# Performance work log

Measured on AMD Instinct MI355X. Metric: run time of the kernel, lower is better.

The kernel has to match this reference:

```python
import jax, jax.numpy as jnp
import numpy as np

B, S, T, F, H, DEPTH = 8, 96, 96, 64, 64, 2


def setup_inputs() -> dict:
    key = jax.random.key(0)
    ks = jax.random.split(key, 10)
    scale = np.float32(1.0 / np.sqrt(H))
    rn = lambda k, sh: jax.random.normal(k, sh, dtype=jnp.float32)
    return {
        "src": rn(ks[0], (B, S, F)),
        "trg": rn(ks[1], (B, T, F)),
        "Wi_x": rn(ks[2], (DEPTH, F, H)) * scale,
        "Wh_x": rn(ks[3], (DEPTH, 2 * H, H)) * scale,
        "b_x": jnp.zeros((DEPTH, H), jnp.float32),
        "Wi_y": rn(ks[4], (DEPTH, F, H)) * scale,
        "Wh_y": rn(ks[5], (DEPTH, 2 * H, H)) * scale,
        "b_y": jnp.zeros((DEPTH, H), jnp.float32),
        "src_lens": jax.random.randint(ks[6], (B,), 1, S + 1),
        "trg_lens": jax.random.randint(ks[7], (B,), 1, T + 1),
    }


def _grid_layer(px, py, Whx, bx, Why, by):
    # px, py: (B, S, T, H) precomputed input projections (x @ Wi).
    # Wavefront recurrence: h_prev = [h_x(i-1,j), h_y(i,j-1)] (zeros at borders),
    # h_x(i,j) = tanh(px + h_prev @ Whx + bx), h_y(i,j) = tanh(py + h_prev @ Why + by).
    Bn, Sn, Tn, Hn = px.shape

    def row_step(hx_above_row, row_in):
        pxr, pyr = row_in  # (T, B, H) each

        def col_step(hy_left, col_in):
            pxc, pyc, hx_above = col_in  # (B, H) each
            h_prev = jnp.concatenate([hx_above, hy_left], axis=-1)  # (B, 2H)
            hx = jnp.tanh(pxc + h_prev @ Whx + bx)
            hy = jnp.tanh(pyc + h_prev @ Why + by)
            return hy, (hx, hy)

        _, (hx_row, hy_row) = jax.lax.scan(
            col_step, jnp.zeros((Bn, Hn), px.dtype), (pxr, pyr, hx_above_row))
        return hx_row, (hx_row, hy_row)

    px_t = jnp.transpose(px, (1, 2, 0, 3))  # (S, T, B, H)
    py_t = jnp.transpose(py, (1, 2, 0, 3))
    _, (hx, hy) = jax.lax.scan(
        row_step, jnp.zeros((Tn, Bn, Hn), px.dtype), (px_t, py_t))
    return jnp.transpose(hx, (2, 0, 1, 3)), jnp.transpose(hy, (2, 0, 1, 3))


def _forward(src, trg, Wi_x, Wh_x, b_x, Wi_y, Wh_y, b_y, src_lens, trg_lens):
    hx = hy = None
    hxs, hys = [], []
    for d in range(DEPTH):
        if d == 0:
            # depth 0: x input depends only on i, y input only on j
            px = jnp.broadcast_to((src @ Wi_x[0])[:, :, None, :], (B, S, T, H))
            py = jnp.broadcast_to((trg @ Wi_y[0])[:, None, :, :], (B, S, T, H))
        else:
            # depth d>0: inputs are previous depth's x/y outputs at the same (i,j)
            px = jnp.einsum('bsth,hk->bstk', hx, Wi_x[d])
            py = jnp.einsum('bsth,hk->bstk', hy, Wi_y[d])
        hx, hy = _grid_layer(px, py, Wh_x[d], b_x[d], Wh_y[d], b_y[d])
        hxs.append(hx)
        hys.append(hy)
    # zero out points outside each sample's (src_len x trg_len) valid grid
    mask = ((jnp.arange(S)[None, :, None] < src_lens[:, None, None])
            & (jnp.arange(T)[None, None, :] < trg_lens[:, None, None]))
    mask = mask[:, :, :, None].astype(src.dtype)  # (B, S, T, 1)
    out = jnp.stack([jnp.stack(hxs), jnp.stack(hys)])  # (2, DEPTH, B, S, T, H)
    return out * mask


_forward_jit = jax.jit(_forward)


def reference(src, trg, Wi_x, Wh_x, b_x, Wi_y, Wh_y, b_y, src_lens, trg_lens):
    return _forward_jit(src, trg, Wi_x, Wh_x, b_x, Wi_y, Wh_y, b_y,
                        src_lens, trg_lens)
```

## Files before the change

kernel.cpp:

```cpp
#include <hip/hip_runtime.h>

typedef unsigned short u16;
typedef unsigned int   u32;
typedef _Float16 f16x8 __attribute__((ext_vector_type(8)));
typedef float  f32x2  __attribute__((ext_vector_type(2)));
typedef float  f32x4  __attribute__((ext_vector_type(4)));
typedef int    i32x4  __attribute__((ext_vector_type(4)));
typedef u32    u32x2  __attribute__((ext_vector_type(2)));

#define Bn 8
#define Sn 96
#define Tn 96
#define Hn 64
#define H2n 128
#define STRB 152
#define ARRB 16384
#define STATEB 131072
#define PXROW 152
#define PXG   (Sn*PXROW)
#define PXBASE STATEB
#define LDSB  (STATEB + 2*PXG)
#define ODS 24320
#define TSTP 2432
#define TSCL 2.885390082f

__device__ __forceinline__ int imax(int a, int b){ return a > b ? a : b; }
__device__ __forceinline__ int imin(int a, int b){ return a < b ? a : b; }

__device__ __forceinline__ u32 pack2f16(float a, float b){
  _Float16 ha = (_Float16)a, hb = (_Float16)b;
  return (u32)__builtin_bit_cast(u16, ha) | ((u32)__builtin_bit_cast(u16, hb) << 16);
}
__device__ __forceinline__ float f16tof(u32 v){
  return (float)__builtin_bit_cast(_Float16, (u16)v);
}
__device__ __forceinline__ float fast_tanh_ps(float zp){
  float e = exp2f(zp);
  return __builtin_fmaf(-2.f, __builtin_amdgcn_rcpf(e + 1.f), 1.f);
}
__device__ __forceinline__ void barrier_lds_only(){
  asm volatile("s_waitcnt vmcnt(63) expcnt(7) lgkmcnt(0)\n\ts_barrier" ::: "memory");
}
__device__ __forceinline__ f16x8 ld_state(const char* p){
  u32x2 a = *(const u32x2*)(p);
  u32x2 b = *(const u32x2*)(p + 8);
  i32x4 v; v[0] = (int)a[0]; v[1] = (int)a[1]; v[2] = (int)b[0]; v[3] = (int)b[1];
  return __builtin_bit_cast(f16x8, v);
}

__global__ __launch_bounds__(64) void proj0_kernel(
  const float* __restrict__ src, const float* __restrict__ trg,
  const float* __restrict__ Wix, const float* __restrict__ Wiy,
  const float* __restrict__ bx, const float* __restrict__ by,
  float* __restrict__ ws)
{
  const int row = blockIdx.x, g = blockIdx.y, b = blockIdx.z;
  const int n = threadIdx.x;
  const float* x = (g == 0) ? (src + (b*Sn + row)*Hn) : (trg + (b*Tn + row)*Hn);
  const float* W = (g == 0) ? Wix : Wiy;
  float a = (g == 0) ? bx[n] : by[n];
  #pragma unroll 8
  for (int f = 0; f < Hn; ++f) a = fmaf(x[f], W[f*Hn + n], a);
  ws[((size_t)(b*2 + g)*Sn + row)*Hn + n] = a * TSCL;
}

__global__ __launch_bounds__(1024, 1) void grid_rnn_fused(
  const float* __restrict__ Whx, const float* __restrict__ Why,
  const float* __restrict__ Wix, const float* __restrict__ Wiy,
  const float* __restrict__ bx,  const float* __restrict__ by,
  const int* __restrict__ src_lens, const int* __restrict__ trg_lens,
  float* __restrict__ out, const float* __restrict__ ws)
{
  extern __shared__ u16 smem[];
  char* const smemc = (char*)smem;
  const int b    = blockIdx.x;
  const int tid  = threadIdx.x;
  const int lane = tid & 63;
  const int wid  = __builtin_amdgcn_readfirstlane(tid >> 6);
  const int q    = lane >> 4;
  const int c    = lane & 15;
  const int dep  = wid & 1;
  const int nh   = (wid >> 1) & 1;
  const int ch   = (wid >> 2) & 1;
  const int g    = wid >> 3;
  const int sl = __builtin_amdgcn_readfirstlane(src_lens[b]);
  const int tl = __builtin_amdgcn_readfirstlane(trg_lens[b]);
  const int NB = sl + tl;

  for (int idx = tid; idx < STATEB/16; idx += 1024) ((i32x4*)smem)[idx] = (i32x4)(0);

  {
    const int gp = tid >> 9;
    const int t5 = tid & 511;
    const float* wsg = ws + (size_t)(b*2 + gp)*Sn*Hn;
    #pragma unroll
    for (int it = 0; it < 6; ++it){
      int w = t5 + it*512;
      int row = w >> 5, pr = w & 31;
      f32x2 v = *(const f32x2*)(wsg + row*64 + pr*2);
      *(u32*)(smemc + PXBASE + gp*PXG + row*PXROW + pr*4) = pack2f16(v[0], v[1]);
    }
  }

  const float* Wh = (g == 0 ? Whx : Why) + dep*H2n*Hn;
  i32x4 whf[4][2];
  #pragma unroll
  for (int kk = 0; kk < 4; ++kk)
    #pragma unroll
    for (int fc = 0; fc < 2; ++fc){
      const int nb = nh*32 + fc*16 + c;
      #pragma unroll
      for (int p = 0; p < 4; ++p){
        float w0 = Wh[(kk*32 + q*8 + 2*p    )*Hn + nb] * TSCL;
        float w1 = Wh[(kk*32 + q*8 + 2*p + 1)*Hn + nb] * TSCL;
        whf[kk][fc][p] = (int)pack2f16(w0, w1);
      }
    }
  const float* Wi = (g == 0 ? Wix : Wiy) + Hn*Hn;
  i32x4 wif[2][2];
  #pragma unroll
  for (int kk = 0; kk < 2; ++kk)
    #pragma unroll
    for (int fc = 0; fc < 2; ++fc){
      const int nb = nh*32 + fc*16 + c;
      #pragma unroll
      for (int p = 0; p < 4; ++p){
        float w0 = Wi[(kk*32 + q*8 + 2*p    )*Hn + nb] * TSCL;
        float w1 = Wi[(kk*32 + q*8 + 2*p + 1)*Hn + nb] * TSCL;
        wif[kk][fc][p] = (int)pack2f16(w0, w1);
      }
    }
  f32x4 bias4[2];
  {
    const float* bb = (g == 0 ? bx : by) + dep*Hn;
    #pragma unroll
    for (int fc = 0; fc < 2; ++fc)
      #pragma unroll
      for (int r4 = 0; r4 < 4; ++r4)
        bias4[fc][r4] = bb[nh*32 + fc*16 + q*4 + r4] * TSCL;
  }
  char* const outb = (char*)(out + (size_t)((g*2 + dep)*Bn + b)*(size_t)(Sn*Tn)*Hn);

  const int plX  = q*16 - c*STRB;
  const int plY  = q*16 + c*STRB;
  const int plP  = g ? plY : plX;
  const int plW  = (g ? c*STRB : -c*STRB) + nh*64 + q*8;
  const int plPx = (g ? -c*PXROW : c*PXROW) + nh*64 + q*8;
  const int plO  = c*ODS + nh*128 + q*16;

  const int depB   = dep*4*ARRB;
  const int basePg = g ? 2*ARRB : 0;
  const int baseWg = depB + (g ? 2*ARRB : 0);

  __syncthreads();

  for (int r = 0; r < NB; ++r){
    const int myd  = r - dep;
    const bool wact = (myd >= 0) && (myd <= NB - 2);
    const int cpB = (r & 1) ? ARRB : 0;
    const int ppB = ARRB - cpB;
    const int i0 = imax(0, myd - (tl - 1));
    const int i1 = imin(sl - 1, myd);
    const int nc = i1 - i0 + 1;
    const int mtiles = (nc + 15) >> 4;
    const int rJ0 = myd - i0, rJm = myd - i1;
    const int aX  = depB + ppB + rJ0*STRB;
    const int loX = depB + ppB + rJm*STRB;
    const int aY  = depB + 2*ARRB + ppB + i0*STRB;
    const int hiY = depB + 2*ARRB + ppB + i1*STRB + 48;
    const int aP  = basePg + ppB + (g ? i0 : rJ0)*STRB;
    const int loP = basePg + ppB + (g ? i0 : rJm)*STRB;
    const int hiP = basePg + ppB + (g ? i1 : rJ0)*STRB + 48;
    const int aW  = baseWg + cpB + (g ? i0 : rJ0)*STRB;
    const int aPx = PXBASE + g*PXG + (g ? rJ0 : i0)*PXROW;
    const int loPx= PXBASE + g*PXG + (g ? rJm : i0)*PXROW;
    const int hiPx= PXBASE + g*PXG + (g ? rJ0 : i1)*PXROW + 88;
    const int sO  = myd*256 + i0*ODS;

    #pragma unroll
    for (int t = 0; t < 3; ++t){
      const int u = ch + 2*t;
      if (!(wact && u < mtiles)) continue;
      const int du = u*TSTP;

      int vX = aX - du + plX; vX = imax(vX, loX);
      int vY = aY + du + plY; vY = imin(vY, hiY);

      f16x8 bvx[2], bvy[2];
      #pragma unroll
      for (int kk = 0; kk < 2; ++kk) bvx[kk] = ld_state(smemc + vX + kk*64);
      #pragma unroll
      for (int kk = 0; kk < 2; ++kk) bvy[kk] = ld_state(smemc + vY + kk*64);

      f32x4 a0, a1;
      if (dep == 0){
        int vp = aPx + (g ? -du : du) + plPx;
        vp = imin(imax(vp, loPx), hiPx);
        u32x2 p0 = *(const u32x2*)(smemc + vp);
        u32x2 p1 = *(const u32x2*)(smemc + vp + 32);
        a0[0] = f16tof(p0[0] & 0xffffu); a0[1] = f16tof(p0[0] >> 16);
        a0[2] = f16tof(p0[1] & 0xffffu); a0[3] = f16tof(p0[1] >> 16);
        a1[0] = f16tof(p1[0] & 0xffffu); a1[1] = f16tof(p1[0] >> 16);
        a1[2] = f16tof(p1[1] & 0xffffu); a1[3] = f16tof(p1[1] >> 16);
      } else {
        a0 = bias4[0]; a1 = bias4[1];
      }
      #pragma unroll
      for (int kk = 0; kk < 2; ++kk){
        a0 = __builtin_amdgcn_mfma_f32_16x16x32_f16(
               __builtin_bit_cast(f16x8, whf[kk][0]), bvx[kk], a0, 0, 0, 0);
        a1 = __builtin_amdgcn_mfma_f32_16x16x32_f16(
               __builtin_bit_cast(f16x8, whf[kk][1]), bvx[kk], a1, 0, 0, 0);
      }
      #pragma unroll
      for (int kk = 0; kk < 2; ++kk){
        a0 = __builtin_amdgcn_mfma_f32_16x16x32_f16(
               __builtin_bit_cast(f16x8, whf[kk+2][0]), bvy[kk], a0, 0, 0, 0);
        a1 = __builtin_amdgcn_mfma_f32_16x16x32_f16(
               __builtin_bit_cast(f16x8, whf[kk+2][1]), bvy[kk], a1, 0, 0, 0);
      }
      if (dep == 1){
        int vP = aP + (g ? du : -du) + plP;
        vP = imin(imax(vP, loP), hiP);
        #pragma unroll
        for (int kk = 0; kk < 2; ++kk){
          f16x8 pv = ld_state(smemc + vP + kk*64);
          a0 = __builtin_amdgcn_mfma_f32_16x16x32_f16(
                 __builtin_bit_cast(f16x8, wif[kk][0]), pv, a0, 0, 0, 0);
          a1 = __builtin_amdgcn_mfma_f32_16x16x32_f16(
                 __builtin_bit_cast(f16x8, wif[kk][1]), pv, a1, 0, 0, 0);
        }
      }
      float h0 = fast_tanh_ps(a0[0]), h1 = fast_tanh_ps(a0[1]);
      float h2 = fast_tanh_ps(a0[2]), h3 = fast_tanh_ps(a0[3]);
      float h4 = fast_tanh_ps(a1[0]), h5 = fast_tanh_ps(a1[1]);
      float h6 = fast_tanh_ps(a1[2]), h7 = fast_tanh_ps(a1[3]);
      if (c < nc - u*16){
        const int vW = aW + (g ? du : -du) + plW;
        u32x2 hp0; hp0[0] = pack2f16(h0, h1); hp0[1] = pack2f16(h2, h3);
        u32x2 hp1; hp1[0] = pack2f16(h4, h5); hp1[1] = pack2f16(h6, h7);
        *(u32x2*)(smemc + vW) = hp0;
        *(u32x2*)(smemc + vW + 32) = hp1;
        char* oa = outb + (u32)(sO + u*(16*ODS) + plO);
        f32x4 ov0 = {h0, h1, h2, h3};
        f32x4 ov1 = {h4, h5, h6, h7};
        *(f32x4*)(oa) = ov0;
        *(f32x4*)(oa + 64) = ov1;
      }
    }
    barrier_lds_only();
  }
}

extern "C" void kernel_launch(void* const* d_in, const int* in_sizes, int n_in,
                              void* d_out, int out_size, void* d_ws, size_t ws_size,
                              hipStream_t stream) {
  (void)in_sizes; (void)n_in; (void)ws_size;
  (void)hipFuncSetAttribute((const void*)grid_rnn_fused,
                            hipFuncAttributeMaxDynamicSharedMemorySize, LDSB);
  (void)hipMemsetAsync(d_out, 0, (size_t)out_size, stream);
  proj0_kernel<<<dim3(Sn, 2, Bn), 64, 0, stream>>>(
      (const float*)d_in[0], (const float*)d_in[1],
      (const float*)d_in[2], (const float*)d_in[5],
      (const float*)d_in[4], (const float*)d_in[7],
      (float*)d_ws);
  grid_rnn_fused<<<dim3(Bn), dim3(1024), LDSB, stream>>>(
      (const float*)d_in[3], (const float*)d_in[6],
      (const float*)d_in[2], (const float*)d_in[5],
      (const float*)d_in[4], (const float*)d_in[7],
      (const int*)d_in[8], (const int*)d_in[9],
      (float*)d_out, (const float*)d_ws);
}
```

Before: 452.1 us.

## Halve block to 512 threads with each wave computing all 64 output columns

Removes the split of output columns across two waves (nh), so each wave now computes all four 16-column fragments of a 16-row tile. The block shrinks from 1024 to 512 threads, and the weight fragments held in registers double per wave. The intent is to halve redundant B-operand state loads and barrier participants per wavefront step, and to give each wave more independent MFMA chains to hide latency. The cost is higher register pressure and fewer waves to hide the serial per-step latency.

```diff
diff --git a/kernel.cpp b/kernel.cpp
--- a/kernel.cpp
+++ b/kernel.cpp
@@ -64,7 +64,7 @@
   ws[((size_t)(b*2 + g)*Sn + row)*Hn + n] = a * TSCL;
 }
 
-__global__ __launch_bounds__(1024, 1) void grid_rnn_fused(
+__global__ __launch_bounds__(512, 1) void grid_rnn_fused(
   const float* __restrict__ Whx, const float* __restrict__ Why,
   const float* __restrict__ Wix, const float* __restrict__ Wiy,
   const float* __restrict__ bx,  const float* __restrict__ by,
@@ -80,22 +80,21 @@
   const int q    = lane >> 4;
   const int c    = lane & 15;
   const int dep  = wid & 1;
-  const int nh   = (wid >> 1) & 1;
-  const int ch   = (wid >> 2) & 1;
-  const int g    = wid >> 3;
+  const int g    = (wid >> 1) & 1;
+  const int ct   = (wid >> 2) & 1;
   const int sl = __builtin_amdgcn_readfirstlane(src_lens[b]);
   const int tl = __builtin_amdgcn_readfirstlane(trg_lens[b]);
   const int NB = sl + tl;
 
-  for (int idx = tid; idx < STATEB/16; idx += 1024) ((i32x4*)smem)[idx] = (i32x4)(0);
+  for (int idx = tid; idx < STATEB/16; idx += 512) ((i32x4*)smem)[idx] = (i32x4)(0);
 
   {
-    const int gp = tid >> 9;
-    const int t5 = tid & 511;
+    const int gp = tid >> 8;
+    const int t5 = tid & 255;
     const float* wsg = ws + (size_t)(b*2 + gp)*Sn*Hn;
     #pragma unroll
-    for (int it = 0; it < 6; ++it){
-      int w = t5 + it*512;
+    for (int it = 0; it < 12; ++it){
+      int w = t5 + it*256;
       int row = w >> 5, pr = w & 31;
       f32x2 v = *(const f32x2*)(wsg + row*64 + pr*2);
       *(u32*)(smemc + PXBASE + gp*PXG + row*PXROW + pr*4) = pack2f16(v[0], v[1]);
@@ -103,12 +102,12 @@
   }
 
   const float* Wh = (g == 0 ? Whx : Why) + dep*H2n*Hn;
-  i32x4 whf[4][2];
+  i32x4 whf[4][4];
   #pragma unroll
   for (int kk = 0; kk < 4; ++kk)
     #pragma unroll
-    for (int fc = 0; fc < 2; ++fc){
-      const int nb = nh*32 + fc*16 + c;
+    for (int fc = 0; fc < 4; ++fc){
+      const int nb = fc*16 + c;
       #pragma unroll
       for (int p = 0; p < 4; ++p){
         float w0 = Wh[(kk*32 + q*8 + 2*p    )*Hn + nb] * TSCL;
@@ -117,12 +116,12 @@
       }
     }
   const float* Wi = (g == 0 ? Wix : Wiy) + Hn*Hn;
-  i32x4 wif[2][2];
+  i32x4 wif[2][4];
   #pragma unroll
   for (int kk = 0; kk < 2; ++kk)
     #pragma unroll
-    for (int fc = 0; fc < 2; ++fc){
-      const int nb = nh*32 + fc*16 + c;
+    for (int fc = 0; fc < 4; ++fc){
+      const int nb = fc*16 + c;
       #pragma unroll
       for (int p = 0; p < 4; ++p){
         float w0 = Wi[(kk*32 + q*8 + 2*p    )*Hn + nb] * TSCL;
@@ -130,23 +129,23 @@
         wif[kk][fc][p] = (int)pack2f16(w0, w1);
       }
     }
-  f32x4 bias4[2];
+  f32x4 bias4[4];
   {
     const float* bb = (g == 0 ? bx : by) + dep*Hn;
     #pragma unroll
-    for (int fc = 0; fc < 2; ++fc)
+    for (int fc = 0; fc < 4; ++fc)
       #pragma unroll
       for (int r4 = 0; r4 < 4; ++r4)
-        bias4[fc][r4] = bb[nh*32 + fc*16 + q*4 + r4] * TSCL;
+        bias4[fc][r4] = bb[fc*16 + q*4 + r4] * TSCL;
   }
   char* const outb = (char*)(out + (size_t)((g*2 + dep)*Bn + b)*(size_t)(Sn*Tn)*Hn);
 
   const int plX  = q*16 - c*STRB;
   const int plY  = q*16 + c*STRB;
   const int plP  = g ? plY : plX;
-  const int plW  = (g ? c*STRB : -c*STRB) + nh*64 + q*8;
-  const int plPx = (g ? -c*PXROW : c*PXROW) + nh*64 + q*8;
-  const int plO  = c*ODS + nh*128 + q*16;
+  const int plW  = (g ? c*STRB : -c*STRB) + q*8;
+  const int plPx = (g ? -c*PXROW : c*PXROW) + q*8;
+  const int plO  = c*ODS + q*16;
 
   const int depB   = dep*4*ARRB;
   const int basePg = g ? 2*ARRB : 0;
@@ -174,12 +173,12 @@
     const int aW  = baseWg + cpB + (g ? i0 : rJ0)*STRB;
     const int aPx = PXBASE + g*PXG + (g ? rJ0 : i0)*PXROW;
     const int loPx= PXBASE + g*PXG + (g ? rJm : i0)*PXROW;
-    const int hiPx= PXBASE + g*PXG + (g ? rJ0 : i1)*PXROW + 88;
+    const int hiPx= PXBASE + g*PXG + (g ? rJ0 : i1)*PXROW + 24;
     const int sO  = myd*256 + i0*ODS;
 
     #pragma unroll
     for (int t = 0; t < 3; ++t){
-      const int u = ch + 2*t;
+      const int u = ct + 2*t;
       if (!(wact && u < mtiles)) continue;
       const int du = u*TSTP;
 
@@ -192,60 +191,57 @@
       #pragma unroll
       for (int kk = 0; kk < 2; ++kk) bvy[kk] = ld_state(smemc + vY + kk*64);
 
-      f32x4 a0, a1;
+      f32x4 a4[4];
       if (dep == 0){
         int vp = aPx + (g ? -du : du) + plPx;
         vp = imin(imax(vp, loPx), hiPx);
-        u32x2 p0 = *(const u32x2*)(smemc + vp);
-        u32x2 p1 = *(const u32x2*)(smemc + vp + 32);
-        a0[0] = f16tof(p0[0] & 0xffffu); a0[1] = f16tof(p0[0] >> 16);
-        a0[2] = f16tof(p0[1] & 0xffffu); a0[3] = f16tof(p0[1] >> 16);
-        a1[0] = f16tof(p1[0] & 0xffffu); a1[1] = f16tof(p1[0] >> 16);
-        a1[2] = f16tof(p1[1] & 0xffffu); a1[3] = f16tof(p1[1] >> 16);
+        #pragma unroll
+        for (int fc = 0; fc < 4; ++fc){
+          u32x2 p0 = *(const u32x2*)(smemc + vp + fc*32);
+          a4[fc][0] = f16tof(p0[0] & 0xffffu); a4[fc][1] = f16tof(p0[0] >> 16);
+          a4[fc][2] = f16tof(p0[1] & 0xffffu); a4[fc][3] = f16tof(p0[1] >> 16);
+        }
       } else {
-        a0 = bias4[0]; a1 = bias4[1];
-      }
-      #pragma unroll
-      for (int kk = 0; kk < 2; ++kk){
-        a0 = __builtin_amdgcn_mfma_f32_16x16x32_f16(
-               __builtin_bit_cast(f16x8, whf[kk][0]), bvx[kk], a0, 0, 0, 0);
-        a1 = __builtin_amdgcn_mfma_f32_16x16x32_f16(
-               __builtin_bit_cast(f16x8, whf[kk][1]), bvx[kk], a1, 0, 0, 0);
-      }
-      #pragma unroll
-      for (int kk = 0; kk < 2; ++kk){
-        a0 = __builtin_amdgcn_mfma_f32_16x16x32_f16(
-               __builtin_bit_cast(f16x8, whf[kk+2][0]), bvy[kk], a0, 0, 0, 0);
-        a1 = __builtin_amdgcn_mfma_f32_16x16x32_f16(
-               __builtin_bit_cast(f16x8, whf[kk+2][1]), bvy[kk], a1, 0, 0, 0);
-      }
+        #pragma unroll
+        for (int fc = 0; fc < 4; ++fc) a4[fc] = bias4[fc];
+      }
+      #pragma unroll
+      for (int kk = 0; kk < 2; ++kk)
+        #pragma unroll
+        for (int fc = 0; fc < 4; ++fc)
+          a4[fc] = __builtin_amdgcn_mfma_f32_16x16x32_f16(
+                     __builtin_bit_cast(f16x8, whf[kk][fc]), bvx[kk], a4[fc], 0, 0, 0);
+      #pragma unroll
+      for (int kk = 0; kk < 2; ++kk)
+        #pragma unroll
+        for (int fc = 0; fc < 4; ++fc)
+          a4[fc] = __builtin_amdgcn_mfma_f32_16x16x32_f16(
+                     __builtin_bit_cast(f16x8, whf[kk+2][fc]), bvy[kk], a4[fc], 0, 0, 0);
       if (dep == 1){
         int vP = aP + (g ? du : -du) + plP;
         vP = imin(imax(vP, loP), hiP);
         #pragma unroll
         for (int kk = 0; kk < 2; ++kk){
           f16x8 pv = ld_state(smemc + vP + kk*64);
-          a0 = __builtin_amdgcn_mfma_f32_16x16x32_f16(
-                 __builtin_bit_cast(f16x8, wif[kk][0]), pv, a0, 0, 0, 0);
-          a1 = __builtin_amdgcn_mfma_f32_16x16x32_f16(
-                 __builtin_bit_cast(f16x8, wif[kk][1]), pv, a1, 0, 0, 0);
+          #pragma unroll
+          for (int fc = 0; fc < 4; ++fc)
+            a4[fc] = __builtin_amdgcn_mfma_f32_16x16x32_f16(
+                       __builtin_bit_cast(f16x8, wif[kk][fc]), pv, a4[fc], 0, 0, 0);
         }
       }
-      float h0 = fast_tanh_ps(a0[0]), h1 = fast_tanh_ps(a0[1]);
-      float h2 = fast_tanh_ps(a0[2]), h3 = fast_tanh_ps(a0[3]);
-      float h4 = fast_tanh_ps(a1[0]), h5 = fast_tanh_ps(a1[1]);
-      float h6 = fast_tanh_ps(a1[2]), h7 = fast_tanh_ps(a1[3]);
       if (c < nc - u*16){
         const int vW = aW + (g ? du : -du) + plW;
-        u32x2 hp0; hp0[0] = pack2f16(h0, h1); hp0[1] = pack2f16(h2, h3);
-        u32x2 hp1; hp1[0] = pack2f16(h4, h5); hp1[1] = pack2f16(h6, h7);
-        *(u32x2*)(smemc + vW) = hp0;
-        *(u32x2*)(smemc + vW + 32) = hp1;
         char* oa = outb + (u32)(sO + u*(16*ODS) + plO);
-        f32x4 ov0 = {h0, h1, h2, h3};
-        f32x4 ov1 = {h4, h5, h6, h7};
-        *(f32x4*)(oa) = ov0;
-        *(f32x4*)(oa + 64) = ov1;
+        #pragma unroll
+        for (int fc = 0; fc < 4; ++fc){
+          float h0 = fast_tanh_ps(a4[fc][0]), h1 = fast_tanh_ps(a4[fc][1]);
+          float h2 = fast_tanh_ps(a4[fc][2]), h3 = fast_tanh_ps(a4[fc][3]);
+          u32x2 hp; hp[0] = pack2f16(h0, h1); hp[1] = pack2f16(h2, h3);
+          *(u32x2*)(smemc + vW + fc*32) = hp;
+          f32x4 ov = {h0, h1, h2, h3};
+          *(f32x4*)(oa + fc*64) = ov;
+        }
+      } else {
       }
     }
     barrier_lds_only();
@@ -264,7 +260,7 @@
       (const float*)d_in[2], (const float*)d_in[5],
       (const float*)d_in[4], (const float*)d_in[7],
       (float*)d_ws);
-  grid_rnn_fused<<<dim3(Bn), dim3(1024), LDSB, stream>>>(
+  grid_rnn_fused<<<dim3(Bn), dim3(512), LDSB, stream>>>(
       (const float*)d_in[3], (const float*)d_in[6],
       (const float*)d_in[2], (const float*)d_in[5],
       (const float*)d_in[4], (const float*)d_in[7],
```

Result: slower. 462.1 us (+2.2%).
